# Performance work log

Measured on AMD Instinct MI355X. Metric: run time of the kernel, lower is better.

The kernel has to match this reference:

```python
import jax, jax.numpy as jnp
import numpy as np


def gcn_conv(x, W, b, src, dst, num_nodes):
    # h = X W  (tiny GEMM)
    h = x @ W
    # symmetric degree normalization with self-loops: D^-1/2 (A+I) D^-1/2
    deg = jax.ops.segment_sum(jnp.ones_like(dst, dtype=h.dtype), dst, num_segments=num_nodes)
    dinv = jnp.where(deg > 0, jax.lax.rsqrt(jnp.maximum(deg, 1e-12)), 0.0)
    norm = dinv[src] * dinv[dst]                      # [E]
    msg = h[src] * norm[:, None]                      # gather + scale, [E, F]
    out = jax.ops.segment_sum(msg, dst, num_segments=num_nodes)  # scatter-add, [N, F]
    return out + b


def reference(x, edge_index, W1, b1, W2, b2):
    num_nodes = x.shape[0]
    # add self-loops once (PyG GCNConv adds them inside each conv; identical edges both layers)
    loop = jnp.arange(num_nodes, dtype=edge_index.dtype)
    src = jnp.concatenate([edge_index[0], loop])
    dst = jnp.concatenate([edge_index[1], loop])
    h = gcn_conv(x, W1, b1, src, dst, num_nodes)
    h = jax.nn.relu(h)
    out = gcn_conv(h, W2, b2, src, dst, num_nodes)
    return out


def setup_inputs() -> dict:
    key = jax.random.key(0)
    k1, k2, k3, k4 = jax.random.split(key, 4)
    N, E, C_in, C_hid, C_out = 100000, 3200000, 128, 16, 128
    x = jax.random.normal(k1, (N, C_in), dtype=jnp.float32)
    edge_index = jax.random.randint(k2, (2, E), 0, N, dtype=jnp.int64)
    W1 = jax.random.normal(k3, (C_in, C_hid), dtype=jnp.float32) * (1.0 / np.sqrt(C_in))
    b1 = jnp.zeros((C_hid,), dtype=jnp.float32)
    W2 = jax.random.normal(k4, (C_hid, C_out), dtype=jnp.float32) * (1.0 / np.sqrt(C_hid))
    b2 = jnp.zeros((C_out,), dtype=jnp.float32)
    return {"x": x, "edge_index": edge_index, "W1": W1, "b1": b1, "W2": W2, "b2": b2}
```

## Files before the change

kernel.cpp:

```cpp
#include <hip/hip_runtime.h>
#include <hip/hip_fp16.h>

typedef _Float16 half8 __attribute__((ext_vector_type(8)));
typedef _Float16 half4 __attribute__((ext_vector_type(4)));
typedef float f32x4 __attribute__((ext_vector_type(4)));
typedef unsigned uint4v __attribute__((ext_vector_type(4)));

#define RANGE    512
#define RSH      9
#define CAP      17408
#define T_TILE   4096

__global__ void init_gcursor(int* __restrict__ gcursor, int NB) {
    int t = blockIdx.x * blockDim.x + threadIdx.x;
    if (t < NB) gcursor[t] = t * CAP;
}


__device__ __forceinline__ void unp8(uint4v v, float* f) {
#pragma unroll
    for (int k = 0; k < 4; ++k) {
        unsigned w = v[k];
        __half2 h2 = *reinterpret_cast<__half2*>(&w);
        float2 t = __half22float2(h2);
        f[2 * k] = t.x; f[2 * k + 1] = t.y;
    }
}

__device__ __forceinline__ void acc8(float* a, uint4v v) {
#pragma unroll
    for (int k = 0; k < 4; ++k) {
        unsigned w = v[k];
        __half2 h2 = *reinterpret_cast<__half2*>(&w);
        float2 t = __half22float2(h2);
        a[2 * k]     += t.x;
        a[2 * k + 1] += t.y;
    }
}

__device__ __forceinline__ uint4v pk8(const float* o) {
    uint4v r;
#pragma unroll
    for (int k = 0; k < 4; ++k) {
        __half2 h2 = __floats2half2_rn(o[2 * k], o[2 * k + 1]);
        r[k] = *reinterpret_cast<unsigned*>(&h2);
    }
    return r;
}


__global__ __launch_bounds__(256) void binpass_gemm1(const int* __restrict__ src,
                                                     const int* __restrict__ dst, int E,
                                                     int* __restrict__ gcursor,
                                                     unsigned* __restrict__ pairbuf,
                                                     int binBlocks,
                                                     const float* __restrict__ x,
                                                     const float* __restrict__ W1,
                                                     __half* __restrict__ g1, int N) {
    if (blockIdx.x >= binBlocks) {
        int wave = threadIdx.x >> 6;
        int lane = threadIdx.x & 63;
        int R0 = (blockIdx.x - binBlocks) * 64 + wave * 16;
        if (R0 >= N) return;
        int m = lane & 15;
        int kb = (lane >> 4) * 8;
        int row = R0 + m;
        int rowc = min(row, N - 1);

        half8 bfrag[4];
#pragma unroll
        for (int kk = 0; kk < 4; ++kk) {
#pragma unroll
            for (int j = 0; j < 8; ++j)
                bfrag[kk][j] = (_Float16)W1[(kk * 32 + kb + j) * 16 + m];
        }
        const float* xr = x + (size_t)rowc * 128;
        float4 u[8];
#pragma unroll
        for (int kk = 0; kk < 4; ++kk) {
            u[2 * kk]     = *reinterpret_cast<const float4*>(xr + kk * 32 + kb);
            u[2 * kk + 1] = *reinterpret_cast<const float4*>(xr + kk * 32 + kb + 4);
        }
        f32x4 acc = {0.f, 0.f, 0.f, 0.f};
#pragma unroll
        for (int kk = 0; kk < 4; ++kk) {
            half8 a;
            a[0] = (_Float16)u[2 * kk].x;     a[1] = (_Float16)u[2 * kk].y;
            a[2] = (_Float16)u[2 * kk].z;     a[3] = (_Float16)u[2 * kk].w;
            a[4] = (_Float16)u[2 * kk + 1].x; a[5] = (_Float16)u[2 * kk + 1].y;
            a[6] = (_Float16)u[2 * kk + 1].z; a[7] = (_Float16)u[2 * kk + 1].w;
            acc = __builtin_amdgcn_mfma_f32_16x16x32_f16(a, bfrag[kk], acc, 0, 0, 0);
        }
#pragma unroll
        for (int i = 0; i < 4; ++i) {
            int r = R0 + (lane >> 4) * 4 + i;
            if (r < N) g1[(size_t)r * 16 + m] = __float2half(acc[i]);
        }
        return;
    }
    __shared__ unsigned sbuf[T_TILE];
    __shared__ int sdst[T_TILE];
    __shared__ int lcount2[512], lplace2[512];
    __shared__ int loff[256], gbase[256];
    int t = threadIdx.x;
    int par = t & 1;
    int base = blockIdx.x * T_TILE;
    int ecount = min(T_TILE, E - base);

    lcount2[2 * t] = 0;
    lcount2[2 * t + 1] = 0;
    __syncthreads();

    unsigned pk[16];
    int bn[16];
#pragma unroll
    for (int k4 = 0; k4 < 4; ++k4) {
        int i = base + (t + k4 * 256) * 4;
        if (i + 3 < E) {
            int4 sv = *reinterpret_cast<const int4*>(src + i);
            int4 dv = *reinterpret_cast<const int4*>(dst + i);
            int ss[4] = {sv.x, sv.y, sv.z, sv.w};
            int dd[4] = {dv.x, dv.y, dv.z, dv.w};
#pragma unroll
            for (int m = 0; m < 4; ++m) {
                int k = k4 * 4 + m;
                bn[k] = dd[m] >> RSH;
                pk[k] = ((unsigned)ss[m] << RSH) | (unsigned)(dd[m] & (RANGE - 1));
                atomicAdd(&lcount2[2 * bn[k] + par], 1);
            }
        } else {
#pragma unroll
            for (int m = 0; m < 4; ++m) {
                int k = k4 * 4 + m;
                int ii = i + m;
                if (ii < E) {
                    int s = src[ii], d = dst[ii];
                    bn[k] = d >> RSH;
                    pk[k] = ((unsigned)s << RSH) | (unsigned)(d & (RANGE - 1));
                    atomicAdd(&lcount2[2 * bn[k] + par], 1);
                } else bn[k] = -1;
            }
        }
    }
    __syncthreads();
    int c0 = lcount2[2 * t], c1 = lcount2[2 * t + 1];
    int c = c0 + c1;
    loff[t] = c;
    __syncthreads();
    for (int off = 1; off < 256; off <<= 1) {
        int u = (t >= off) ? loff[t - off] : 0;
        __syncthreads();
        loff[t] += u;
        __syncthreads();
    }
    int ex = loff[t] - c;
    lplace2[2 * t] = ex;
    lplace2[2 * t + 1] = ex + c0;
    if (c > 0) gbase[t] = atomicAdd(&gcursor[t], c) - ex;
    __syncthreads();
#pragma unroll
    for (int k = 0; k < 16; ++k) {
        if (bn[k] >= 0) {
            int b = bn[k];
            int pos = atomicAdd(&lplace2[2 * b + par], 1);
            sbuf[pos] = pk[k];
            sdst[pos] = gbase[b] + pos;
        }
    }
    __syncthreads();
    for (int i = t; i < ecount; i += 256) {
        pairbuf[sdst[i]] = sbuf[i];
    }
}


__global__ __launch_bounds__(1024) void bucket_build(const unsigned* __restrict__ pairbuf,
                                                     const int* __restrict__ gcursor,
                                                     int NB, int N, int E,
                                                     int* __restrict__ rowptr,
                                                     float* __restrict__ dinv,
                                                     int* __restrict__ eidx,
                                                     __half* __restrict__ g1,
                                                     __half* __restrict__ g2) {
    __shared__ unsigned spair[CAP];
    __shared__ int lcnt[RANGE];
    __shared__ int lsc[RANGE];
    __shared__ int sscan[256];
    int b = blockIdx.x, t = threadIdx.x;

    if (t < 256) sscan[t] = (t < NB) ? (gcursor[t] - t * CAP) : 0;
    if (t < RANGE) lcnt[t] = 0;
    __syncthreads();
    for (int off = 1; off < 256; off <<= 1) {
        int u = (t >= off && t < 256) ? sscan[t - off] : 0;
        __syncthreads();
        if (t < 256) sscan[t] += u;
        __syncthreads();
    }
    int gb = (b == 0) ? 0 : sscan[b - 1];
    int cnt = gcursor[b] - b * CAP;
    const unsigned* pb = pairbuf + (size_t)b * CAP;

    for (int i = t; i < cnt; i += 1024) {
        unsigned p = pb[i];
        spair[i] = p;
        atomicAdd(&lcnt[p & (RANGE - 1)], 1);
    }
    __syncthreads();
    if (t < RANGE) lsc[t] = lcnt[t];
    __syncthreads();
    for (int off = 1; off < RANGE; off <<= 1) {
        int u = (t >= off && t < RANGE) ? lsc[t - off] : 0;
        __syncthreads();
        if (t < RANGE) lsc[t] += u;
        __syncthreads();
    }
    if (t < RANGE) {
        int ex = lsc[t] - lcnt[t];
        int node = b * RANGE + t;
        if (node < N) {
            rowptr[node] = gb + ex;
            float di = rsqrtf((float)lcnt[t] + 1.0f);
            dinv[node] = di;
            __half* gr = g1 + (size_t)node * 16;
            uint4v v0 = *reinterpret_cast<const uint4v*>(gr);
            uint4v v1 = *reinterpret_cast<const uint4v*>(gr + 8);
            float f[8];
            unp8(v0, f);
#pragma unroll
            for (int k = 0; k < 8; ++k) f[k] *= di;
            *reinterpret_cast<uint4v*>(gr) = pk8(f);
            unp8(v1, f);
#pragma unroll
            for (int k = 0; k < 8; ++k) f[k] *= di;
            *reinterpret_cast<uint4v*>(gr + 8) = pk8(f);
        } else if (node == N) {
            uint4v z = {0u, 0u, 0u, 0u};
            *reinterpret_cast<uint4v*>(g1 + (size_t)N * 16)     = z;
            *reinterpret_cast<uint4v*>(g1 + (size_t)N * 16 + 8) = z;
            *reinterpret_cast<uint4v*>(g2 + (size_t)N * 16)     = z;
            *reinterpret_cast<uint4v*>(g2 + (size_t)N * 16 + 8) = z;
        }
        if (b == 0 && t == 0) rowptr[N] = E;
    }
    __syncthreads();
    if (t < RANGE) lsc[t] = gb + (lsc[t] - lcnt[t]);
    __syncthreads();
    for (int i = t; i < cnt; i += 1024) {
        unsigned p = spair[i];
        int pos = atomicAdd(&lsc[p & (RANGE - 1)], 1);
        eidx[pos] = (int)(p >> RSH);
    }
}


__global__ __launch_bounds__(256) void gather1_kernel(const int* __restrict__ rowptr,
                                                      const int* __restrict__ eidx,
                                                      const __half* __restrict__ g1,
                                                      const float* __restrict__ dinv,
                                                      const float* __restrict__ b1,
                                                      __half* __restrict__ g2, int N) {
    int gid = blockIdx.x * blockDim.x + threadIdx.x;
    int d = gid >> 4;
    if (d >= N) return;
    int sub = threadIdx.x & 15;
    int h = sub & 1, es = sub >> 1;
    int f0 = h * 8;
    int lo = rowptr[d], hi = rowptr[d + 1];
    float di = dinv[d];
    uint4v svh = *reinterpret_cast<const uint4v*>(g1 + (size_t)d * 16 + f0);

    float a[8] = {0, 0, 0, 0, 0, 0, 0, 0};
    for (int j = lo + es; j < hi; j += 64) {
        int idx[8];
#pragma unroll
        for (int k = 0; k < 8; ++k) {
            int jj = j + 8 * k;
            idx[k] = (jj < hi) ? eidx[jj] : N;
        }
        uint4v v[8];
#pragma unroll
        for (int k = 0; k < 8; ++k)
            v[k] = *reinterpret_cast<const uint4v*>(g1 + (size_t)idx[k] * 16 + f0);
#pragma unroll
        for (int k = 0; k < 8; ++k) acc8(a, v[k]);
    }
#pragma unroll
    for (int k = 0; k < 8; ++k) {
        a[k] += __shfl_xor(a[k], 2);
        a[k] += __shfl_xor(a[k], 4);
        a[k] += __shfl_xor(a[k], 8);
    }
    if (es == 0) {
        float sf[8];
        unp8(svh, sf);
        f32x4 bb0 = *reinterpret_cast<const f32x4*>(b1 + f0);
        f32x4 bb1 = *reinterpret_cast<const f32x4*>(b1 + f0 + 4);
        float o[8];
#pragma unroll
        for (int k = 0; k < 4; ++k) {
            o[k]     = fmaxf(di * (a[k] + sf[k]) + bb0[k], 0.0f) * di;
            o[k + 4] = fmaxf(di * (a[k + 4] + sf[k + 4]) + bb1[k], 0.0f) * di;
        }
        *reinterpret_cast<uint4v*>(g2 + (size_t)d * 16 + f0) = pk8(o);
    }
}


__global__ __launch_bounds__(256) void gather2_kernel(const int* __restrict__ rowptr,
                                                      const int* __restrict__ eidx,
                                                      const __half* __restrict__ g2,
                                                      const float* __restrict__ dinv,
                                                      __half* __restrict__ g3, int N) {
    int gid = blockIdx.x * blockDim.x + threadIdx.x;
    int d = gid >> 4;
    if (d >= N) return;
    int sub = threadIdx.x & 15;
    int h = sub & 1, es = sub >> 1;
    int f0 = h * 8;
    int lo = rowptr[d], hi = rowptr[d + 1];
    float di = dinv[d];
    uint4v svh = *reinterpret_cast<const uint4v*>(g2 + (size_t)d * 16 + f0);

    float a[8] = {0, 0, 0, 0, 0, 0, 0, 0};
    for (int j = lo + es; j < hi; j += 64) {
        int idx[8];
#pragma unroll
        for (int k = 0; k < 8; ++k) {
            int jj = j + 8 * k;
            idx[k] = (jj < hi) ? eidx[jj] : N;
        }
        uint4v v[8];
#pragma unroll
        for (int k = 0; k < 8; ++k)
            v[k] = *reinterpret_cast<const uint4v*>(g2 + (size_t)idx[k] * 16 + f0);
#pragma unroll
        for (int k = 0; k < 8; ++k) acc8(a, v[k]);
    }
#pragma unroll
    for (int k = 0; k < 8; ++k) {
        a[k] += __shfl_xor(a[k], 2);
        a[k] += __shfl_xor(a[k], 4);
        a[k] += __shfl_xor(a[k], 8);
    }
    if (es == 0) {
        float sf[8];
        unp8(svh, sf);
        float o[8];
#pragma unroll
        for (int k = 0; k < 8; ++k) o[k] = di * (a[k] + sf[k]);
        *reinterpret_cast<uint4v*>(g3 + (size_t)d * 16 + f0) = pk8(o);
    }
}


__global__ __launch_bounds__(256) void gemm2_mfma(const __half* __restrict__ g3,
                                                  const float* __restrict__ W2,
                                                  const float* __restrict__ b2,
                                                  float* __restrict__ out, int N) {
    int wave = threadIdx.x >> 6;
    int lane = threadIdx.x & 63;
    int R0 = blockIdx.x * 64 + wave * 16;
    if (R0 >= N) return;
    int nl = lane & 15;
    int q = lane >> 4;
    int row = R0 + nl;
    int rowc = min(row, N - 1);

    half4 afrag = *reinterpret_cast<const half4*>(g3 + (size_t)rowc * 16 + q * 4);

    f32x4 dacc[8];
#pragma unroll
    for (int ct = 0; ct < 8; ++ct) {
        half4 bfrag;
#pragma unroll
        for (int jj = 0; jj < 4; ++jj)
            bfrag[jj] = (_Float16)W2[(q * 4 + jj) * 128 + ct * 16 + nl];
        f32x4 z = {0.f, 0.f, 0.f, 0.f};
        dacc[ct] = __builtin_amdgcn_mfma_f32_16x16x16f16(afrag, bfrag, z, 0, 0, 0);
    }

    float bias[8];
#pragma unroll
    for (int ct = 0; ct < 8; ++ct) bias[ct] = b2[ct * 16 + nl];

    int rbase = R0 + q * 4;
#pragma unroll
    for (int i = 0; i < 4; ++i) {
        int r = rbase + i;
        if (r < N) {
            float* orow = out + (size_t)r * 128 + nl;
#pragma unroll
            for (int ct = 0; ct < 8; ++ct) orow[ct * 16] = dacc[ct][i] + bias[ct];
        }
    }
}


extern "C" void kernel_launch(void* const* d_in, const int* in_sizes, int n_in,
                              void* d_out, int out_size, void* d_ws, size_t ws_size,
                              hipStream_t stream) {
    const float* x  = (const float*)d_in[0];
    const int*   ei = (const int*)d_in[1];
    const float* W1 = (const float*)d_in[2];
    const float* b1 = (const float*)d_in[3];
    const float* W2 = (const float*)d_in[4];
    const float* b2 = (const float*)d_in[5];
    float* out = (float*)d_out;

    const int N = in_sizes[0] / 128;
    const int E = in_sizes[1] / 2;
    const int* src = ei;
    const int* dst = ei + E;
    const int NB = (N + RANGE - 1) / RANGE;

    unsigned* pairbuf = (unsigned*)d_ws;
    int* gcursor = (int*)(pairbuf + (size_t)NB * CAP);
    int* rowptr  = gcursor + NB;
    int* eidx    = rowptr + (N + 1);
    float* dinv  = (float*)(eidx + E);
    __half* g1 = (__half*)(dinv + N);
    __half* g2 = g1 + 16 * (N + 1);
    __half* g3 = g2 + 16 * (N + 1);

    const int B = 256;
    const int binBlocks  = (E + T_TILE - 1) / T_TILE;
    const int gemmBlocks = (N + 63) / 64;
    init_gcursor<<<1, B, 0, stream>>>(gcursor, NB);
    binpass_gemm1<<<binBlocks + gemmBlocks, B, 0, stream>>>(src, dst, E, gcursor, pairbuf,
                                                            binBlocks, x, W1, g1, N);
    bucket_build<<<NB, 1024, 0, stream>>>(pairbuf, gcursor, NB, N, E, rowptr, dinv, eidx, g1, g2);
    gather1_kernel<<<(N * 16 + B - 1) / B, B, 0, stream>>>(rowptr, eidx, g1, dinv, b1, g2, N);
    gather2_kernel<<<(N * 16 + B - 1) / B, B, 0, stream>>>(rowptr, eidx, g2, dinv, g3, N);
    gemm2_mfma<<<gemmBlocks, B, 0, stream>>>(g3, W2, b2, out, N);
}
```

Measured before the change: 124.3 us.

## Move GEMM1 from binning kernel into bucket-build kernel, add separate scale pass

The x@W1 MFMA blocks move out of the binning kernel and are appended as extra blocks to the bucket-build kernel, using 1024-thread blocks that each cover 256 rows. Because g1 may not be finished when a bucket block computes dinv, the dinv scaling of g1 becomes its own small kernel launched afterwards. The aim is to rebalance the stages: the binning pass no longer shares the GPU with the GEMM, and the GEMM overlaps the shared-memory-heavy bucket blocks instead. The cost is one extra launch and an extra read and write of g1.

```diff
diff --git a/kernel.cpp b/kernel.cpp
--- a/kernel.cpp
+++ b/kernel.cpp
@@ -49,55 +49,10 @@
 }
 
 
-__global__ __launch_bounds__(256) void binpass_gemm1(const int* __restrict__ src,
-                                                     const int* __restrict__ dst, int E,
-                                                     int* __restrict__ gcursor,
-                                                     unsigned* __restrict__ pairbuf,
-                                                     int binBlocks,
-                                                     const float* __restrict__ x,
-                                                     const float* __restrict__ W1,
-                                                     __half* __restrict__ g1, int N) {
-    if (blockIdx.x >= binBlocks) {
-        int wave = threadIdx.x >> 6;
-        int lane = threadIdx.x & 63;
-        int R0 = (blockIdx.x - binBlocks) * 64 + wave * 16;
-        if (R0 >= N) return;
-        int m = lane & 15;
-        int kb = (lane >> 4) * 8;
-        int row = R0 + m;
-        int rowc = min(row, N - 1);
-
-        half8 bfrag[4];
-#pragma unroll
-        for (int kk = 0; kk < 4; ++kk) {
-#pragma unroll
-            for (int j = 0; j < 8; ++j)
-                bfrag[kk][j] = (_Float16)W1[(kk * 32 + kb + j) * 16 + m];
-        }
-        const float* xr = x + (size_t)rowc * 128;
-        float4 u[8];
-#pragma unroll
-        for (int kk = 0; kk < 4; ++kk) {
-            u[2 * kk]     = *reinterpret_cast<const float4*>(xr + kk * 32 + kb);
-            u[2 * kk + 1] = *reinterpret_cast<const float4*>(xr + kk * 32 + kb + 4);
-        }
-        f32x4 acc = {0.f, 0.f, 0.f, 0.f};
-#pragma unroll
-        for (int kk = 0; kk < 4; ++kk) {
-            half8 a;
-            a[0] = (_Float16)u[2 * kk].x;     a[1] = (_Float16)u[2 * kk].y;
-            a[2] = (_Float16)u[2 * kk].z;     a[3] = (_Float16)u[2 * kk].w;
-            a[4] = (_Float16)u[2 * kk + 1].x; a[5] = (_Float16)u[2 * kk + 1].y;
-            a[6] = (_Float16)u[2 * kk + 1].z; a[7] = (_Float16)u[2 * kk + 1].w;
-            acc = __builtin_amdgcn_mfma_f32_16x16x32_f16(a, bfrag[kk], acc, 0, 0, 0);
-        }
-#pragma unroll
-        for (int i = 0; i < 4; ++i) {
-            int r = R0 + (lane >> 4) * 4 + i;
-            if (r < N) g1[(size_t)r * 16 + m] = __float2half(acc[i]);
-        }
-        return;
-    }
+__global__ __launch_bounds__(256) void binpass(const int* __restrict__ src,
+                                               const int* __restrict__ dst, int E,
+                                               int* __restrict__ gcursor,
+                                               unsigned* __restrict__ pairbuf) {
     __shared__ unsigned sbuf[T_TILE];
     __shared__ int sdst[T_TILE];
     __shared__ int lcount2[512], lplace2[512];
@@ -174,14 +129,57 @@
 }
 
 
-__global__ __launch_bounds__(1024) void bucket_build(const unsigned* __restrict__ pairbuf,
+__global__ __launch_bounds__(1024) void bucket_gemm1(const unsigned* __restrict__ pairbuf,
                                                      const int* __restrict__ gcursor,
                                                      int NB, int N, int E,
                                                      int* __restrict__ rowptr,
                                                      float* __restrict__ dinv,
                                                      int* __restrict__ eidx,
+                                                     const float* __restrict__ x,
+                                                     const float* __restrict__ W1,
                                                      __half* __restrict__ g1,
                                                      __half* __restrict__ g2) {
+    if (blockIdx.x >= NB) {
+        int wave = threadIdx.x >> 6;
+        int lane = threadIdx.x & 63;
+        int R0 = (blockIdx.x - NB) * 256 + wave * 16;
+        if (R0 >= N) return;
+        int m = lane & 15;
+        int kb = (lane >> 4) * 8;
+        int row = R0 + m;
+        int rowc = min(row, N - 1);
+
+        half8 bfrag[4];
+#pragma unroll
+        for (int kk = 0; kk < 4; ++kk) {
+#pragma unroll
+            for (int j = 0; j < 8; ++j)
+                bfrag[kk][j] = (_Float16)W1[(kk * 32 + kb + j) * 16 + m];
+        }
+        const float* xr = x + (size_t)rowc * 128;
+        float4 u[8];
+#pragma unroll
+        for (int kk = 0; kk < 4; ++kk) {
+            u[2 * kk]     = *reinterpret_cast<const float4*>(xr + kk * 32 + kb);
+            u[2 * kk + 1] = *reinterpret_cast<const float4*>(xr + kk * 32 + kb + 4);
+        }
+        f32x4 acc = {0.f, 0.f, 0.f, 0.f};
+#pragma unroll
+        for (int kk = 0; kk < 4; ++kk) {
+            half8 a;
+            a[0] = (_Float16)u[2 * kk].x;     a[1] = (_Float16)u[2 * kk].y;
+            a[2] = (_Float16)u[2 * kk].z;     a[3] = (_Float16)u[2 * kk].w;
+            a[4] = (_Float16)u[2 * kk + 1].x; a[5] = (_Float16)u[2 * kk + 1].y;
+            a[6] = (_Float16)u[2 * kk + 1].z; a[7] = (_Float16)u[2 * kk + 1].w;
+            acc = __builtin_amdgcn_mfma_f32_16x16x32_f16(a, bfrag[kk], acc, 0, 0, 0);
+        }
+#pragma unroll
+        for (int i = 0; i < 4; ++i) {
+            int r = R0 + (lane >> 4) * 4 + i;
+            if (r < N) g1[(size_t)r * 16 + m] = __float2half(acc[i]);
+        }
+        return;
+    }
     __shared__ unsigned spair[CAP];
     __shared__ int lcnt[RANGE];
     __shared__ int lsc[RANGE];
@@ -220,20 +218,7 @@
         int node = b * RANGE + t;
         if (node < N) {
             rowptr[node] = gb + ex;
-            float di = rsqrtf((float)lcnt[t] + 1.0f);
-            dinv[node] = di;
-            __half* gr = g1 + (size_t)node * 16;
-            uint4v v0 = *reinterpret_cast<const uint4v*>(gr);
-            uint4v v1 = *reinterpret_cast<const uint4v*>(gr + 8);
-            float f[8];
-            unp8(v0, f);
-#pragma unroll
-            for (int k = 0; k < 8; ++k) f[k] *= di;
-            *reinterpret_cast<uint4v*>(gr) = pk8(f);
-            unp8(v1, f);
-#pragma unroll
-            for (int k = 0; k < 8; ++k) f[k] *= di;
-            *reinterpret_cast<uint4v*>(gr + 8) = pk8(f);
+            dinv[node] = rsqrtf((float)lcnt[t] + 1.0f);
         } else if (node == N) {
             uint4v z = {0u, 0u, 0u, 0u};
             *reinterpret_cast<uint4v*>(g1 + (size_t)N * 16)     = z;
@@ -251,6 +236,21 @@
         int pos = atomicAdd(&lsc[p & (RANGE - 1)], 1);
         eidx[pos] = (int)(p >> RSH);
     }
+}
+
+
+__global__ __launch_bounds__(256) void scale_g1(__half* __restrict__ g1,
+                                                const float* __restrict__ dinv, int N) {
+    int gid = blockIdx.x * blockDim.x + threadIdx.x;
+    if (gid >= N * 2) return;
+    int node = gid >> 1, f0 = (gid & 1) * 8;
+    float di = dinv[node];
+    uint4v v = *reinterpret_cast<const uint4v*>(g1 + (size_t)node * 16 + f0);
+    float f[8];
+    unp8(v, f);
+#pragma unroll
+    for (int k = 0; k < 8; ++k) f[k] *= di;
+    *reinterpret_cast<uint4v*>(g1 + (size_t)node * 16 + f0) = pk8(f);
 }
 
 
@@ -424,13 +424,15 @@
     __half* g3 = g2 + 16 * (N + 1);
 
     const int B = 256;
-    const int binBlocks  = (E + T_TILE - 1) / T_TILE;
-    const int gemmBlocks = (N + 63) / 64;
+    const int binBlocks   = (E + T_TILE - 1) / T_TILE;
+    const int gemm1Blocks = (N + 255) / 256;
+    const int gemm2Blocks = (N + 63) / 64;
     init_gcursor<<<1, B, 0, stream>>>(gcursor, NB);
-    binpass_gemm1<<<binBlocks + gemmBlocks, B, 0, stream>>>(src, dst, E, gcursor, pairbuf,
-                                                            binBlocks, x, W1, g1, N);
-    bucket_build<<<NB, 1024, 0, stream>>>(pairbuf, gcursor, NB, N, E, rowptr, dinv, eidx, g1, g2);
+    binpass<<<binBlocks, B, 0, stream>>>(src, dst, E, gcursor, pairbuf);
+    bucket_gemm1<<<NB + gemm1Blocks, 1024, 0, stream>>>(pairbuf, gcursor, NB, N, E,
+                                                        rowptr, dinv, eidx, x, W1, g1, g2);
+    scale_g1<<<(N * 2 + B - 1) / B, B, 0, stream>>>(g1, dinv, N);
     gather1_kernel<<<(N * 16 + B - 1) / B, B, 0, stream>>>(rowptr, eidx, g1, dinv, b1, g2, N);
     gather2_kernel<<<(N * 16 + B - 1) / B, B, 0, stream>>>(rowptr, eidx, g2, dinv, g3, N);
-    gemm2_mfma<<<gemmBlocks, B, 0, stream>>>(g3, W2, b2, out, N);
-}
+    gemm2_mfma<<<gemm2Blocks, B, 0, stream>>>(g3, W2, b2, out, N);
+}
```

Measured after the change: 125.1 us. No clear change (+0.7%).
